# Kernel tuning notes

Hardware: AMD Instinct MI355X
Metric: run time of the kernel (lower is better)

Reference implementation:

```python
import jax, jax.numpy as jnp
import numpy as np

N_HEADS = 16

def setup_inputs() -> dict:
    key = jax.random.key(0)
    ks = jax.random.split(key, 9)
    B, L, D = 4, 2048, 1024
    s = D ** -0.5
    return {
        "x": jax.random.normal(ks[0], (B, L, D), dtype=jnp.float32),
        "Wq": jax.random.normal(ks[1], (D, D), dtype=jnp.float32) * s,
        "bq": jax.random.normal(ks[2], (D,), dtype=jnp.float32) * 0.02,
        "Wk": jax.random.normal(ks[3], (D, D), dtype=jnp.float32) * s,
        "bk": jax.random.normal(ks[4], (D,), dtype=jnp.float32) * 0.02,
        "Wv": jax.random.normal(ks[5], (D, D), dtype=jnp.float32) * s,
        "bv": jax.random.normal(ks[6], (D,), dtype=jnp.float32) * 0.02,
        "Wo": jax.random.normal(ks[7], (D, D), dtype=jnp.float32) * s,
        "bo": jax.random.normal(ks[8], (D,), dtype=jnp.float32) * 0.02,
    }

def reference(x, Wq, bq, Wk, bk, Wv, bv, Wo, bo):
    B, L, D = x.shape
    H = N_HEADS
    hd = D // H
    scale = hd ** -0.5
    # torch Linear: y = x @ W.T + b
    q = (x @ Wq.T + bq).reshape(B, L, H, hd)
    k = (x @ Wk.T + bk).reshape(B, L, H, hd)
    v = (x @ Wv.T + bv).reshape(B, L, H, hd)
    # scores [B,H,L,L]
    qk = jnp.einsum('bqhd,bkhd->bhqk', q, k) * scale
    causal = jnp.tril(jnp.ones((L, L), dtype=bool))
    qk = jnp.where(causal[None, None, :, :], qk, -jnp.inf)
    attn = jax.nn.softmax(qk, axis=-1)
    out = jnp.einsum('bhqk,bkhd->bqhd', attn, v).reshape(B, L, D)
    return out @ Wo.T + bo
```

## Files before the change

kernel.cpp:

```cpp
#include <hip/hip_runtime.h>
#include <hip/hip_bf16.h>
#include <math.h>

#define Bsz 4
#define Lsz 2048
#define Dsz 1024
#define Hn 16
#define HDsz 64
#define NQT 16

typedef __attribute__((ext_vector_type(8))) short short8;
typedef __attribute__((ext_vector_type(4))) float floatx4;
typedef unsigned short ushort_t;

__device__ __forceinline__ void load_lds_16B(const void* g, void* l) {
    __builtin_amdgcn_global_load_lds(
        (const __attribute__((address_space(1))) unsigned int*)g,
        (__attribute__((address_space(3))) unsigned int*)l, 16, 0, 0);
}

__device__ inline void cvt_store(float* p, size_t i, float v) { p[i] = v; }
__device__ inline void cvt_store(__hip_bfloat16* p, size_t i, float v) {
    p[i] = __float2bfloat16(v);
}

__device__ inline ushort_t f2bf_raw(float f) {
    __hip_bfloat16 b = __float2bfloat16(f);
    return *reinterpret_cast<ushort_t*>(&b);
}

__device__ inline float bf2f_raw(ushort_t u) {
    union { unsigned int i; float f; } c;
    c.i = ((unsigned int)u) << 16;
    return c.f;
}

__device__ __forceinline__ float fast_exp2(float x) {
#if __has_builtin(__builtin_amdgcn_exp2f)
    return __builtin_amdgcn_exp2f(x);
#else
    return exp2f(x);
#endif
}

__device__ __forceinline__ unsigned pk_bf16_rhu(float p0, float p1) {
    return __builtin_amdgcn_perm(__builtin_bit_cast(unsigned, p1) + 0x8000u,
                                 __builtin_bit_cast(unsigned, p0) + 0x8000u,
                                 0x07060302u);
}

__global__ __launch_bounds__(256) void f2b(const float* __restrict__ in,
                                           __hip_bfloat16* __restrict__ out,
                                           int n) {
    int i = (blockIdx.x * 256 + threadIdx.x) * 4;
    if (i >= n) return;
    float4 v = *(const float4*)(in + i);
    out[i + 0] = __float2bfloat16(v.x);
    out[i + 1] = __float2bfloat16(v.y);
    out[i + 2] = __float2bfloat16(v.z);
    out[i + 3] = __float2bfloat16(v.w);
}

template <typename TO, bool QKV>
__global__ __launch_bounds__(256) void gemm_bt_mfma(
    const ushort_t* __restrict__ A, const ushort_t* __restrict__ W,
    const float* __restrict__ b0, const float* __restrict__ b1,
    const float* __restrict__ b2, TO* __restrict__ C, int M, int N, int K) {
    __shared__ ushort_t As[128 * 32];
    __shared__ ushort_t Bs[128 * 32];

    const int t = threadIdx.x;
    const int wave = t >> 6, lane = t & 63;
    const int m0 = blockIdx.y * 128, n0 = blockIdx.x * 128;
    const int wm = (wave & 1) * 64, wn = (wave >> 1) * 64;
    const int lmod = lane & 15, quad = lane >> 4;

    floatx4 acc[4][4] = {};

    for (int k0 = 0; k0 < K; k0 += 32) {
#pragma unroll
        for (int p = 0; p < 2; p++) {
            int chunk = t + p * 256;
            int r = chunk >> 2;
            int c8 = (chunk & 3) * 8;
            load_lds_16B(A + (size_t)(m0 + r) * K + k0 + c8, &As[chunk * 8]);
            load_lds_16B(W + (size_t)(n0 + r) * K + k0 + c8, &Bs[chunk * 8]);
        }
        __syncthreads();

        short8 af[4], bf_[4];
#pragma unroll
        for (int i = 0; i < 4; i++) {
            af[i] = *(const short8*)&As[(wm + i * 16 + lmod) * 32 + quad * 8];
            bf_[i] = *(const short8*)&Bs[(wn + i * 16 + lmod) * 32 + quad * 8];
        }
#pragma unroll
        for (int i = 0; i < 4; i++)
#pragma unroll
            for (int j = 0; j < 4; j++)
                acc[i][j] = __builtin_amdgcn_mfma_f32_16x16x32_bf16(
                    af[i], bf_[j], acc[i][j], 0, 0, 0);
        __syncthreads();
    }

    const int sec = n0 >> 10;
    const float* bp = QKV ? (sec == 0 ? b0 : (sec == 1 ? b1 : b2)) : b0;
    TO* Cb = QKV ? (C + (size_t)sec * M * 1024) : C;
    const int Nout = QKV ? 1024 : N;
    const float sc = (QKV && sec == 0) ? 0.1803368801111204f : 1.0f;

#pragma unroll
    for (int i = 0; i < 4; i++) {
        int gm = m0 + wm + i * 16 + quad * 4;
#pragma unroll
        for (int j = 0; j < 4; j++) {
            int gn = n0 + wn + j * 16 + lmod;
            int cn = QKV ? (gn & 1023) : gn;
            float b = bp[cn];
#pragma unroll
            for (int r = 0; r < 4; r++)
                cvt_store(Cb, (size_t)(gm + r) * Nout + cn,
                          (acc[i][j][r] + b) * sc);
        }
    }
}

__global__ __launch_bounds__(256) void attn_mfma(
    const ushort_t* __restrict__ q, const ushort_t* __restrict__ k,
    const ushort_t* __restrict__ v, ushort_t* __restrict__ Opart,
    float* __restrict__ lpart) {
    __shared__ ushort_t Ks[64 * 64];
    __shared__ ushort_t Vts[64 * 64];
    __shared__ ushort_t Ps[4][32 * 64];

    const int t = threadIdx.x;
    const int wave = t >> 6, lane = t & 63;
    const int lmod = lane & 15, quad = lane >> 4;
    const int p = blockIdx.x & 7, s = blockIdx.x >> 3;
    const int bh = blockIdx.y;
    const int b = bh >> 4, h = bh & 15;
    const size_t base = ((size_t)b * Lsz) * Dsz + h * HDsz;

    const int vrp = t & 31, vcg = t >> 5;
    ushort_t* Pw = (ushort_t*)Ps[wave];
    const int lm7 = lmod & 7;

#pragma unroll 1
    for (int seg = 0; seg < 2; seg++) {
        const int qtile = seg == 0 ? (NQT - 1 - p) : p;
        const int q0 = qtile * 128;
        const int Th = qtile + 1;
        const int kt0 = s * Th, kt1 = kt0 + Th;

        short8 aq[2][2];
#pragma unroll
        for (int g = 0; g < 2; g++) {
            const ushort_t* qp = q + base +
                                 (size_t)(q0 + wave * 32 + g * 16 + lmod) * Dsz +
                                 quad * 8;
            aq[g][0] = *(const short8*)(qp);
            aq[g][1] = *(const short8*)(qp + 32);
        }

        floatx4 Oacc[2][4] = {};
        float lsum[2] = {0.f, 0.f};

        for (int kt = kt0; kt < kt1; kt++) {
            __syncthreads();

#pragma unroll
            for (int pp = 0; pp < 2; pp++) {
                int slot = t + pp * 256;
                int row = slot >> 3, c8 = slot & 7;
                int gc8 = c8 ^ (row & 7);
                load_lds_16B(k + base + (size_t)(kt * 64 + row) * Dsz + gc8 * 8,
                             &Ks[slot * 8]);
            }
            {
                const ushort_t* v0p =
                    v + base + (size_t)(kt * 64 + 2 * vrp) * Dsz + vcg * 8;
                uint4 v0 = *(const uint4*)v0p;
                uint4 v1 = *(const uint4*)(v0p + Dsz);
                unsigned vv0[4] = {v0.x, v0.y, v0.z, v0.w};
                unsigned vv1[4] = {v1.x, v1.y, v1.z, v1.w};
                const int kk = 2 * vrp;
                const int kc8 = kk >> 3, klo = kk & 7;
#pragma unroll
                for (int jj = 0; jj < 4; jj++) {
                    int d0 = vcg * 8 + 2 * jj;
                    unsigned lo =
                        __builtin_amdgcn_perm(vv1[jj], vv0[jj], 0x05040100u);
                    unsigned hi =
                        __builtin_amdgcn_perm(vv1[jj], vv0[jj], 0x07060302u);
                    *(unsigned*)&Vts[d0 * 64 + (kc8 ^ (d0 & 7)) * 8 + klo] = lo;
                    int d1 = d0 + 1;
                    *(unsigned*)&Vts[d1 * 64 + (kc8 ^ (d1 & 7)) * 8 + klo] = hi;
                }
            }
            __syncthreads();

            floatx4 St[2][4] = {};
#pragma unroll
            for (int nt = 0; nt < 4; nt++) {
                int key = nt * 16 + lmod;
#pragma unroll
                for (int ks = 0; ks < 2; ks++) {
                    int sc8 = (ks * 4 + quad) ^ (key & 7);
                    short8 kf = *(const short8*)&Ks[(key * 8 + sc8) * 8];
#pragma unroll
                    for (int g = 0; g < 2; g++)
                        St[g][nt] = __builtin_amdgcn_mfma_f32_16x16x32_bf16(
                            kf, aq[g][ks], St[g][nt], 0, 0, 0);
                }
            }

            const bool need_mask = (kt >= 2 * qtile);
#pragma unroll
            for (int g = 0; g < 2; g++) {
                int qg = q0 + wave * 32 + g * 16 + lmod;
#pragma unroll
                for (int nt = 0; nt < 4; nt++) {
                    int k0g = kt * 64 + nt * 16 + quad * 4;
                    float p0 = fast_exp2(St[g][nt][0]);
                    float p1 = fast_exp2(St[g][nt][1]);
                    float p2 = fast_exp2(St[g][nt][2]);
                    float p3 = fast_exp2(St[g][nt][3]);
                    if (need_mask) {
                        if (k0g + 0 > qg) p0 = 0.f;
                        if (k0g + 1 > qg) p1 = 0.f;
                        if (k0g + 2 > qg) p2 = 0.f;
                        if (k0g + 3 > qg) p3 = 0.f;
                    }
                    lsum[g] += ((p0 + p1) + (p2 + p3));
                    uint2 w;
                    w.x = pk_bf16_rhu(p0, p1);
                    w.y = pk_bf16_rhu(p2, p3);
                    int c8 = nt * 2 + (quad >> 1);
                    int sc8 = c8 ^ lm7;
                    *(uint2*)&Pw[((g * 16 + lmod) * 8 + sc8) * 8 +
                                 (quad & 1) * 4] = w;
                }
            }

            short8 ap[2][2];
#pragma unroll
            for (int g = 0; g < 2; g++)
#pragma unroll
                for (int ks = 0; ks < 2; ks++) {
                    int sc8 = (ks * 4 + quad) ^ lm7;
                    ap[g][ks] =
                        *(const short8*)&Pw[((g * 16 + lmod) * 8 + sc8) * 8];
                }
#pragma unroll
            for (int on = 0; on < 4; on++) {
                int d = on * 16 + lmod;
#pragma unroll
                for (int ks = 0; ks < 2; ks++) {
                    int sc8 = (ks * 4 + quad) ^ (d & 7);
                    short8 bv = *(const short8*)&Vts[(d * 8 + sc8) * 8];
#pragma unroll
                    for (int g = 0; g < 2; g++)
                        Oacc[g][on] = __builtin_amdgcn_mfma_f32_16x16x32_bf16(
                            ap[g][ks], bv, Oacc[g][on], 0, 0, 0);
                }
            }
        }

#pragma unroll
        for (int g = 0; g < 2; g++) {
            lsum[g] += __shfl_xor(lsum[g], 16);
            lsum[g] += __shfl_xor(lsum[g], 32);
        }

        const size_t rec = ((size_t)bh * NQT + qtile) * 2 + s;
        ushort_t* Orec = Opart + rec * (128 * 64);
        float* lrec = lpart + rec * 128;
#pragma unroll
        for (int g = 0; g < 2; g++) {
            if (quad == 0) lrec[wave * 32 + g * 16 + lmod] = lsum[g];
#pragma unroll
            for (int r = 0; r < 4; r++) {
                int row = wave * 32 + g * 16 + quad * 4 + r;
#pragma unroll
                for (int on = 0; on < 4; on++) {
                    int d = on * 16 + lmod;
                    Orec[row * 64 + d] = f2bf_raw(Oacc[g][on][r]);
                }
            }
        }
    }
}

__global__ __launch_bounds__(256) void attn_combine(
    const ushort_t* __restrict__ Opart, const float* __restrict__ lpart,
    ushort_t* __restrict__ ao) {
    int gidx = blockIdx.x * 256 + threadIdx.x;
    int rowglob = gidx >> 3;
    int c8 = (gidx & 7) * 8;
    int bh = rowglob >> 11;
    int r11 = rowglob & 2047;
    int qtile = r11 >> 7, row = r11 & 127;

    size_t rec0 = ((size_t)bh * NQT + qtile) * 2;
    const ushort_t* O0 = Opart + (rec0 + 0) * (128 * 64) + row * 64 + c8;
    const ushort_t* O1 = Opart + (rec0 + 1) * (128 * 64) + row * 64 + c8;
    float l = lpart[(rec0 + 0) * 128 + row] + lpart[(rec0 + 1) * 128 + row];
    float inv = 1.0f / l;

    short8 a = *(const short8*)O0;
    short8 bvec = *(const short8*)O1;
    short8 o;
#pragma unroll
    for (int j = 0; j < 8; j++) {
        float vv = (bf2f_raw((ushort_t)a[j]) + bf2f_raw((ushort_t)bvec[j])) * inv;
        o[j] = (short)f2bf_raw(vv);
    }
    int b = bh >> 4, h = bh & 15;
    int qg = qtile * 128 + row;
    *(short8*)&ao[((size_t)(b * Lsz + qg)) * Dsz + h * HDsz + c8] = o;
}

extern "C" void kernel_launch(void* const* d_in, const int* in_sizes, int n_in,
                              void* d_out, int out_size, void* d_ws,
                              size_t ws_size, hipStream_t stream) {
    const size_t elems = (size_t)Bsz * Lsz * Dsz;
    const size_t welem = (size_t)Dsz * Dsz;
    const size_t nrec = (size_t)Bsz * Hn * NQT * 2;
    const size_t opart_e = nrec * 128 * 64;
    const size_t need = (5 * elems + 4 * welem + opart_e) * 2 + nrec * 128 * 4;
    if (ws_size < need) return;

    const float* x = (const float*)d_in[0];
    const float* Wq = (const float*)d_in[1];
    const float* bq = (const float*)d_in[2];
    const float* Wk = (const float*)d_in[3];
    const float* bk = (const float*)d_in[4];
    const float* Wv = (const float*)d_in[5];
    const float* bv = (const float*)d_in[6];
    const float* Wo = (const float*)d_in[7];
    const float* bo = (const float*)d_in[8];
    float* out = (float*)d_out;

    __hip_bfloat16* xb = (__hip_bfloat16*)d_ws;
    __hip_bfloat16* q = xb + elems;
    __hip_bfloat16* k = q + elems;
    __hip_bfloat16* v = k + elems;
    __hip_bfloat16* ao = v + elems;
    __hip_bfloat16* Wqb = ao + elems;
    __hip_bfloat16* Wkb = Wqb + welem;
    __hip_bfloat16* Wvb = Wkb + welem;
    __hip_bfloat16* Wob = Wvb + welem;
    ushort_t* Opart = (ushort_t*)(Wob + welem);
    float* lpart = (float*)(Opart + opart_e);

    const int M = Bsz * Lsz, N = Dsz, K = Dsz;

    f2b<<<(int)(elems / 4 + 255) / 256, 256, 0, stream>>>(x, xb, (int)elems);
    f2b<<<(int)(welem / 4 + 255) / 256, 256, 0, stream>>>(Wq, Wqb, (int)welem);
    f2b<<<(int)(welem / 4 + 255) / 256, 256, 0, stream>>>(Wk, Wkb, (int)welem);
    f2b<<<(int)(welem / 4 + 255) / 256, 256, 0, stream>>>(Wv, Wvb, (int)welem);
    f2b<<<(int)(welem / 4 + 255) / 256, 256, 0, stream>>>(Wo, Wob, (int)welem);

    gemm_bt_mfma<__hip_bfloat16, true><<<dim3(3 * N / 128, M / 128), 256, 0,
                                         stream>>>(
        (const ushort_t*)xb, (const ushort_t*)Wqb, bq, bk, bv, q, M, 3 * N, K);

    attn_mfma<<<dim3(16, Bsz * Hn), 256, 0, stream>>>(
        (const ushort_t*)q, (const ushort_t*)k, (const ushort_t*)v, Opart,
        lpart);

    attn_combine<<<(int)(elems / 8 / 256), 256, 0, stream>>>(Opart, lpart,
                                                             (ushort_t*)ao);

    gemm_bt_mfma<float, false><<<dim3(N / 128, M / 128), 256, 0, stream>>>(
        (const ushort_t*)ao, (const ushort_t*)Wob, bo, bo, bo, out, M, N, K);
}
```

Baseline: 295.4 us.

## Double-buffer K/V tiles in attention kernel to overlap loads with MFMA

Makes the K and V shared-memory tiles double-buffered and prefetches the next key tile while the current one is computed. K goes through async global-to-LDS loads and V through registers, with the V transpose written after the softmax step. This drops one barrier per iteration and aims to hide global load latency behind the matrix work. In exchange it doubles the K/V LDS footprint, which may lower occupancy, and keeps extra live registers for the prefetched V.

```diff
diff --git a/kernel.cpp b/kernel.cpp
--- a/kernel.cpp
+++ b/kernel.cpp
@@ -129,8 +129,8 @@
     const ushort_t* __restrict__ q, const ushort_t* __restrict__ k,
     const ushort_t* __restrict__ v, ushort_t* __restrict__ Opart,
     float* __restrict__ lpart) {
-    __shared__ ushort_t Ks[64 * 64];
-    __shared__ ushort_t Vts[64 * 64];
+    __shared__ ushort_t Ks[2][64 * 64];
+    __shared__ ushort_t Vts[2][64 * 64];
     __shared__ ushort_t Ps[4][32 * 64];
 
     const int t = threadIdx.x;
@@ -145,6 +145,38 @@
     ushort_t* Pw = (ushort_t*)Ps[wave];
     const int lm7 = lmod & 7;
 
+    auto stageK = [&](int kt, int bi) {
+#pragma unroll
+        for (int pp = 0; pp < 2; pp++) {
+            int slot = t + pp * 256;
+            int row = slot >> 3, c8 = slot & 7;
+            int gc8 = c8 ^ (row & 7);
+            load_lds_16B(k + base + (size_t)(kt * 64 + row) * Dsz + gc8 * 8,
+                         &Ks[bi][slot * 8]);
+        }
+    };
+    auto loadV = [&](int kt, uint4& r0, uint4& r1) {
+        const ushort_t* v0p =
+            v + base + (size_t)(kt * 64 + 2 * vrp) * Dsz + vcg * 8;
+        r0 = *(const uint4*)v0p;
+        r1 = *(const uint4*)(v0p + Dsz);
+    };
+    auto writeV = [&](int bi, uint4 r0, uint4 r1) {
+        unsigned vv0[4] = {r0.x, r0.y, r0.z, r0.w};
+        unsigned vv1[4] = {r1.x, r1.y, r1.z, r1.w};
+        const int kk = 2 * vrp;
+        const int kc8 = kk >> 3, klo = kk & 7;
+#pragma unroll
+        for (int jj = 0; jj < 4; jj++) {
+            int d0 = vcg * 8 + 2 * jj;
+            unsigned lo = __builtin_amdgcn_perm(vv1[jj], vv0[jj], 0x05040100u);
+            unsigned hi = __builtin_amdgcn_perm(vv1[jj], vv0[jj], 0x07060302u);
+            *(unsigned*)&Vts[bi][d0 * 64 + (kc8 ^ (d0 & 7)) * 8 + klo] = lo;
+            int d1 = d0 + 1;
+            *(unsigned*)&Vts[bi][d1 * 64 + (kc8 ^ (d1 & 7)) * 8 + klo] = hi;
+        }
+    };
+
 #pragma unroll 1
     for (int seg = 0; seg < 2; seg++) {
         const int qtile = seg == 0 ? (NQT - 1 - p) : p;
@@ -165,39 +197,24 @@
         floatx4 Oacc[2][4] = {};
         float lsum[2] = {0.f, 0.f};
 
+        uint4 vr0, vr1;
+        stageK(kt0, 0);
+        loadV(kt0, vr0, vr1);
+        writeV(0, vr0, vr1);
+        __syncthreads();
+
+#pragma unroll 1
         for (int kt = kt0; kt < kt1; kt++) {
-            __syncthreads();
-
-#pragma unroll
-            for (int pp = 0; pp < 2; pp++) {
-                int slot = t + pp * 256;
-                int row = slot >> 3, c8 = slot & 7;
-                int gc8 = c8 ^ (row & 7);
-                load_lds_16B(k + base + (size_t)(kt * 64 + row) * Dsz + gc8 * 8,
-                             &Ks[slot * 8]);
-            }
-            {
-                const ushort_t* v0p =
-                    v + base + (size_t)(kt * 64 + 2 * vrp) * Dsz + vcg * 8;
-                uint4 v0 = *(const uint4*)v0p;
-                uint4 v1 = *(const uint4*)(v0p + Dsz);
-                unsigned vv0[4] = {v0.x, v0.y, v0.z, v0.w};
-                unsigned vv1[4] = {v1.x, v1.y, v1.z, v1.w};
-                const int kk = 2 * vrp;
-                const int kc8 = kk >> 3, klo = kk & 7;
-#pragma unroll
-                for (int jj = 0; jj < 4; jj++) {
-                    int d0 = vcg * 8 + 2 * jj;
-                    unsigned lo =
-                        __builtin_amdgcn_perm(vv1[jj], vv0[jj], 0x05040100u);
-                    unsigned hi =
-                        __builtin_amdgcn_perm(vv1[jj], vv0[jj], 0x07060302u);
-                    *(unsigned*)&Vts[d0 * 64 + (kc8 ^ (d0 & 7)) * 8 + klo] = lo;
-                    int d1 = d0 + 1;
-                    *(unsigned*)&Vts[d1 * 64 + (kc8 ^ (d1 & 7)) * 8 + klo] = hi;
-                }
-            }
-            __syncthreads();
+            const int cur = (kt - kt0) & 1;
+            const int nxt = cur ^ 1;
+            const bool pf = (kt + 1 < kt1);
+            const ushort_t* Kc = Ks[cur];
+            const ushort_t* Vc = Vts[cur];
+
+            if (pf) {
+                stageK(kt + 1, nxt);
+                loadV(kt + 1, vr0, vr1);
+            }
 
             floatx4 St[2][4] = {};
 #pragma unroll
@@ -206,7 +223,7 @@
 #pragma unroll
                 for (int ks = 0; ks < 2; ks++) {
                     int sc8 = (ks * 4 + quad) ^ (key & 7);
-                    short8 kf = *(const short8*)&Ks[(key * 8 + sc8) * 8];
+                    short8 kf = *(const short8*)&Kc[(key * 8 + sc8) * 8];
 #pragma unroll
                     for (int g = 0; g < 2; g++)
                         St[g][nt] = __builtin_amdgcn_mfma_f32_16x16x32_bf16(
@@ -242,6 +259,8 @@
                 }
             }
 
+            if (pf) writeV(nxt, vr0, vr1);
+
             short8 ap[2][2];
 #pragma unroll
             for (int g = 0; g < 2; g++)
@@ -257,13 +276,15 @@
 #pragma unroll
                 for (int ks = 0; ks < 2; ks++) {
                     int sc8 = (ks * 4 + quad) ^ (d & 7);
-                    short8 bv = *(const short8*)&Vts[(d * 8 + sc8) * 8];
+                    short8 bv = *(const short8*)&Vc[(d * 8 + sc8) * 8];
 #pragma unroll
                     for (int g = 0; g < 2; g++)
                         Oacc[g][on] = __builtin_amdgcn_mfma_f32_16x16x32_bf16(
                             ap[g][ks], bv, Oacc[g][on], 0, 0, 0);
                 }
             }
+
+            __syncthreads();
         }
 
 #pragma unroll
```

After: 299.8 us. No clear change (+1.5%).
